# Kernel tuning notes

Measured on AMD Instinct MI355X. Metric: run time of the kernel, lower is better.

The kernel has to match this reference:

```python
import jax, jax.numpy as jnp
import numpy as np

K = 3        # kernel_size
PAD = 1      # padding
STRIDE = 1   # stride (must be 1: module asserts offset HxW == input HxW)
DIL = 1      # dilation


def _bilinear_gather(x, py, px):
    """x: (B,C,H,W); py,px: (B,KK,Ho,Wo) float sample coords.
    Returns (B,C,KK,Ho,Wo), zero outside bounds (DCNv2 semantics)."""
    B, C, H, W = x.shape
    y0 = jnp.floor(py); x0 = jnp.floor(px)
    wy1 = py - y0; wy0 = 1.0 - wy1
    wx1 = px - x0; wx0 = 1.0 - wx1
    flat = x.reshape(B, C, H * W)

    def gather(yi, xi):
        valid = (yi >= 0) & (yi < H) & (xi >= 0) & (xi < W)
        yc = jnp.clip(yi, 0, H - 1).astype(jnp.int32)
        xc = jnp.clip(xi, 0, W - 1).astype(jnp.int32)
        idx = (yc * W + xc).reshape(B, 1, -1)                      # (B,1,KK*Ho*Wo)
        g = jnp.take_along_axis(flat, jnp.broadcast_to(idx, (B, C, idx.shape[-1])), axis=2)
        g = g.reshape(B, C, *yi.shape[1:])                          # (B,C,KK,Ho,Wo)
        return jnp.where(valid[:, None], g, 0.0)

    v00 = gather(y0, x0)
    v01 = gather(y0, x0 + 1)
    v10 = gather(y0 + 1, x0)
    v11 = gather(y0 + 1, x0 + 1)
    wy0 = wy0[:, None]; wy1 = wy1[:, None]; wx0 = wx0[:, None]; wx1 = wx1[:, None]
    return wy0 * (wx0 * v00 + wx1 * v01) + wy1 * (wx0 * v10 + wx1 * v11)


def dcn_v2(x, coord_offset, coord_weight, weight, bias):
    B, C, H, W = x.shape
    O = weight.shape[0]
    KK = K * K
    # offset channels ordered (k, [y,x]) per DCNv2 layout
    offs = coord_offset.reshape(B, KK, 2, H, W)
    oy, ox = offs[:, :, 0], offs[:, :, 1]
    ky, kx = jnp.meshgrid(jnp.arange(K), jnp.arange(K), indexing='ij')
    ky = ky.reshape(KK); kx = kx.reshape(KK)
    # base sampling grid for each output pixel / kernel tap: (KK,H,W)
    py = (jnp.arange(H) * STRIDE - PAD)[None, :, None] + (ky * DIL)[:, None, None]
    px = (jnp.arange(W) * STRIDE - PAD)[None, None, :] + (kx * DIL)[:, None, None]
    py = py.astype(x.dtype)[None] + oy   # (B,KK,H,W)
    px = px.astype(x.dtype)[None] + ox
    sampled = _bilinear_gather(x, py, px)              # (B,C,KK,H,W)
    sampled = sampled * coord_weight[:, None]          # modulation mask
    out = jnp.einsum('bckhw,ock->bohw', sampled, weight.reshape(O, C, KK))
    return out + bias[None, :, None, None]


def setup_inputs() -> dict:
    key = jax.random.key(0)
    k1, k2, k3, k4, k5 = jax.random.split(key, 5)
    B, C, O, H, W = 8, 256, 256, 64, 64
    return {
        'input': jax.random.normal(k1, (B, C, H, W), dtype=jnp.float32),
        'coord_offset': jax.random.normal(k2, (B, 2 * K * K, H, W), dtype=jnp.float32),
        'coord_weight': jax.random.uniform(k3, (B, K * K, H, W), dtype=jnp.float32),
        'weight': jax.random.normal(k4, (O, C, K, K), dtype=jnp.float32) * 0.02,
        'bias': jax.random.normal(k5, (O,), dtype=jnp.float32) * 0.01,
    }


def reference(input, coord_offset, coord_weight, weight, bias):
    return dcn_v2(input, coord_offset, coord_weight, weight, bias)
```

## Files before the change

kernel.cpp:

```cpp
#include <hip/hip_runtime.h>
#include <hip/hip_bf16.h>
#include <stdint.h>

typedef _Float16 f16_t;
typedef f16_t f16x8 __attribute__((ext_vector_type(8)));
typedef float f32x4 __attribute__((ext_vector_type(4)));

__device__ inline void lgkm_barrier() {
    __builtin_amdgcn_s_waitcnt(0xC07F);
    __builtin_amdgcn_s_barrier();
}

__global__ __launch_bounds__(512) void k_prep(const float* __restrict__ x,
                                              const float* __restrict__ w,
                                              f16_t* __restrict__ xt,
                                              f16_t* __restrict__ Wp) {
    __shared__ __align__(16) float lw[9216];
    const int t = threadIdx.x;
    if (blockIdx.x < 512) {
        const int b = blockIdx.x >> 6;
        const int y = blockIdx.x & 63;
        const float* src = x + ((size_t)(b * 256) * 64 + y) * 64;
        const int x4 = (t & 15) * 4;
        const int c0 = (t >> 4) * 8;
        float4 v[8];
#pragma unroll
        for (int e = 0; e < 8; ++e)
            v[e] = *(const float4*)(src + (size_t)(c0 + e) * 4096 + x4);
        f16_t* dst = xt + ((size_t)(b * 64 + y) * 64) * 256;
#pragma unroll
        for (int j = 0; j < 4; ++j) {
            f16x8 o;
#pragma unroll
            for (int e = 0; e < 8; ++e) {
                const float f = (j == 0) ? v[e].x : (j == 1) ? v[e].y
                              : (j == 2) ? v[e].z : v[e].w;
                o[e] = (f16_t)f;
            }
            *(f16x8*)(dst + (x4 + j) * 256 + c0) = o;
        }
    } else {
        const int o0 = (blockIdx.x - 512) * 4;
        const float4* srcw = (const float4*)(w + (size_t)o0 * 2304);
#pragma unroll
        for (int i = 0; i < 5; ++i) {
            const int idx = t + 512 * i;
            if (idx < 2304) ((float4*)lw)[idx] = srcw[idx];
        }
        __syncthreads();
#pragma unroll
        for (int i = 0; i < 3; ++i) {
            const int u = t + 512 * i;
            if (u < 1152) {
                const int o = u / 288, r = u - o * 288;
                const int kb2 = r >> 3, rr = r & 7;
                const int s = rr >> 2, qq = rr & 3;
                const int kk = kb2 >> 2, cp = kb2 & 3;
                f16x8 vv;
#pragma unroll
                for (int e = 0; e < 8; ++e) {
                    const int c = cp * 64 + s * 32 + qq * 8 + e;
                    vv[e] = (f16_t)lw[o * 2304 + c * 9 + kk];
                }
                *(f16x8*)(Wp + ((size_t)(kb2 * 2 + s) * 256 + o0 + o) * 32 + qq * 8) = vv;
            }
        }
    }
}

__global__ __launch_bounds__(512, 4) void k_dcn(
    const f16_t* __restrict__ xt, const f16_t* __restrict__ Wp,
    const float* __restrict__ coff, const float* __restrict__ cwm,
    const float* __restrict__ bias, float* __restrict__ out) {

    __shared__ __align__(16) f16_t sS[2][64 * 64];
    __shared__ __align__(16) int2 sT[9 * 64 * 4];

    const int blk = blockIdx.x;
    const int b  = blk & 7;
    const int h  = blk >> 3;
    const int t = threadIdx.x;
    const int wv = t >> 6;
    const int lane = t & 63;
    const int mg = wv >> 1;
    const int ng = wv & 1;

    const int p = t >> 3;
    const int q = t & 7;

    const int fr = lane & 15;
    const int quad = lane >> 4;
    const int swz = fr & 7;

    for (int u = t; u < 576; u += 512) {
        const int kk = u >> 6, wpx = u & 63;
        float oy = coff[((size_t)(b * 18 + kk * 2 + 0) * 64 + h) * 64 + wpx];
        float ox = coff[((size_t)(b * 18 + kk * 2 + 1) * 64 + h) * 64 + wpx];
        float m  = cwm [((size_t)(b * 9 + kk) * 64 + h) * 64 + wpx];
        float py = (float)(h - 1 + (kk / 3)) + oy;
        float px = (float)(wpx - 1 + (kk % 3)) + ox;
        float fy = floorf(py), fx = floorf(px);
        int y0 = (int)fy, x0 = (int)fx;
        int y1 = y0 + 1,  x1 = x0 + 1;
        float wy1 = py - fy, wx1 = px - fx;
        float wy0 = 1.0f - wy1, wx0 = 1.0f - wx1;
        bool vy0 = (y0 >= 0) && (y0 < 64), vy1 = (y1 >= 0) && (y1 < 64);
        bool vx0 = (x0 >= 0) && (x0 < 64), vx1 = (x1 >= 0) && (x1 < 64);
        int yc0 = min(max(y0, 0), 63), yc1 = min(max(y1, 0), 63);
        int xc0 = min(max(x0, 0), 63), xc1 = min(max(x1, 0), 63);
        const int base = b * 4096;
        float cw[4];
        int   ca[4];
        cw[0] = (vy0 && vx0) ? wy0 * wx0 * m : 0.0f;
        cw[1] = (vy0 && vx1) ? wy0 * wx1 * m : 0.0f;
        cw[2] = (vy1 && vx0) ? wy1 * wx0 * m : 0.0f;
        cw[3] = (vy1 && vx1) ? wy1 * wx1 * m : 0.0f;
        ca[0] = (base + yc0 * 64 + xc0) * 512;
        ca[1] = (base + yc0 * 64 + xc1) * 512;
        ca[2] = (base + yc1 * 64 + xc0) * 512;
        ca[3] = (base + yc1 * 64 + xc1) * 512;
#pragma unroll
        for (int c = 0; c < 4; ++c) {
            unsigned short ws = __builtin_bit_cast(unsigned short, (f16_t)cw[c]);
            sT[(kk * 64 + wpx) * 4 + c] = make_int2(ca[c], (int)ws);
        }
    }
    __syncthreads();

    const f16_t* wA = Wp + (mg * 64 + fr) * 32 + quad * 8;
    f16_t* const swb0 = &sS[0][p * 64 + ((q ^ (p & 7)) * 8)];
    const int qb = q * 16;
    const char* xb = (const char*)xt;

    f32x4 acc[4][2] = {};
    f16x8 aC[4][2];
    f16x8 g0, g1, g2, g3;
    int4 t0, t1;

    auto loadA = [&](int it) {
        const f16_t* wn = wA + (size_t)it * 16384;
#pragma unroll
        for (int mt = 0; mt < 4; ++mt) {
            aC[mt][0] = *(const f16x8*)(wn + mt * 512);
            aC[mt][1] = *(const f16x8*)(wn + 8192 + mt * 512);
        }
    };

    auto gather_issue = [&](int it) {
        const int kk = it >> 2, cp = it & 3;
        const int4* tp = (const int4*)&sT[(kk * 64 + p) * 4];
        t0 = tp[0];
        t1 = tp[1];
        const int cb = cp * 128 + qb;
        g0 = *(const f16x8*)(xb + (t0.x + cb));
        g1 = *(const f16x8*)(xb + (t0.z + cb));
        g2 = *(const f16x8*)(xb + (t1.x + cb));
        g3 = *(const f16x8*)(xb + (t1.z + cb));
    };

    auto combine_write = [&](int buf) {
        f16_t w0 = __builtin_bit_cast(f16_t, (unsigned short)t0.y);
        f16_t w1 = __builtin_bit_cast(f16_t, (unsigned short)t0.w);
        f16_t w2 = __builtin_bit_cast(f16_t, (unsigned short)t1.y);
        f16_t w3 = __builtin_bit_cast(f16_t, (unsigned short)t1.w);
        f16x8 w0v = {w0, w0, w0, w0, w0, w0, w0, w0};
        f16x8 w1v = {w1, w1, w1, w1, w1, w1, w1, w1};
        f16x8 w2v = {w2, w2, w2, w2, w2, w2, w2, w2};
        f16x8 w3v = {w3, w3, w3, w3, w3, w3, w3, w3};
        f16x8 ov = g0 * w0v + g1 * w1v + g2 * w2v + g3 * w3v;
        *(f16x8*)(swb0 + buf * 4096) = ov;
    };

    auto do_mfma = [&](int cur) {
        const f16_t* sb = &sS[cur][ng * 2048];
#pragma unroll
        for (int s = 0; s < 2; ++s) {
            const int coffe = ((s * 4 + quad) ^ swz) * 8;
            f16x8 bb[2];
#pragma unroll
            for (int nt = 0; nt < 2; ++nt)
                bb[nt] = *(const f16x8*)(sb + (nt * 16 + fr) * 64 + coffe);
#pragma unroll
            for (int mt = 0; mt < 4; ++mt)
#pragma unroll
                for (int nt = 0; nt < 2; ++nt)
                    acc[mt][nt] = __builtin_amdgcn_mfma_f32_16x16x32_f16(
                        aC[mt][s], bb[nt], acc[mt][nt], 0, 0, 0);
        }
    };

    gather_issue(0);
    combine_write(0);
    loadA(0);
    lgkm_barrier();

#pragma unroll 2
    for (int it = 0; it < 35; ++it) {
        const int cur = it & 1;
        gather_issue(it + 1);
        __builtin_amdgcn_sched_barrier(0);
        do_mfma(cur);
        __builtin_amdgcn_sched_barrier(0);
        combine_write(1 - cur);
        loadA(it + 1);
        lgkm_barrier();
    }
    do_mfma(1);

    const int rowq = quad * 4;
#pragma unroll
    for (int mt = 0; mt < 4; ++mt) {
#pragma unroll
        for (int r = 0; r < 4; ++r) {
            const int og = mg * 64 + mt * 16 + rowq + r;
            const float bs = bias[og];
            float* opn = out + ((size_t)(b * 256 + og) * 64 + h) * 64 + ng * 32;
#pragma unroll
            for (int nt = 0; nt < 2; ++nt) {
                opn[nt * 16 + fr] = acc[mt][nt][r] + bs;
            }
        }
    }
}

extern "C" void kernel_launch(void* const* d_in, const int* in_sizes, int n_in,
                              void* d_out, int out_size, void* d_ws, size_t ws_size,
                              hipStream_t stream) {
    const float* x    = (const float*)d_in[0];
    const float* coff = (const float*)d_in[1];
    const float* cwm  = (const float*)d_in[2];
    const float* wgt  = (const float*)d_in[3];
    const float* bias = (const float*)d_in[4];
    float* out = (float*)d_out;

    f16_t* xt = (f16_t*)d_ws;
    f16_t* Wp = xt + (size_t)8 * 64 * 64 * 256;

    k_prep<<<576, 512, 0, stream>>>(x, wgt, xt, Wp);
    k_dcn <<<512, 512, 0, stream>>>(xt, Wp, coff, cwm, bias, out);
}
```

Before: 178.8 us.

## Repartition MFMA waves to 32x64 tiles and double-buffer weight registers

Changes the per-wave output tile from 64 output channels by 32 pixels to 32 channels by 64 pixels, so each wave holds half as many weight fragments and reads all four B tiles from shared memory. The loop is manually unrolled by two with ping-pong register sets (aA/aB), so the next weight fragments load before the current MFMAs run. Gather table entries are now reloaded from LDS only once per kernel tap, and MFMA sections get raised wave priority via s_setprio. In exchange, each wave issues more LDS B reads, and the loop tail runs one redundant weight load.

```diff
diff --git a/kernel.cpp b/kernel.cpp
--- a/kernel.cpp
+++ b/kernel.cpp
@@ -82,8 +82,6 @@
     const int t = threadIdx.x;
     const int wv = t >> 6;
     const int lane = t & 63;
-    const int mg = wv >> 1;
-    const int ng = wv & 1;
 
     const int p = t >> 3;
     const int q = t & 7;
@@ -127,30 +125,31 @@
     }
     __syncthreads();
 
-    const f16_t* wA = Wp + (mg * 64 + fr) * 32 + quad * 8;
+    const f16_t* wA = Wp + (wv * 32 + fr) * 32 + quad * 8;
     f16_t* const swb0 = &sS[0][p * 64 + ((q ^ (p & 7)) * 8)];
     const int qb = q * 16;
     const char* xb = (const char*)xt;
 
-    f32x4 acc[4][2] = {};
-    f16x8 aC[4][2];
+    f32x4 acc[2][4] = {};
+    f16x8 aA[2][2], aB[2][2];
     f16x8 g0, g1, g2, g3;
     int4 t0, t1;
 
-    auto loadA = [&](int it) {
+    auto loadA = [&](int it, f16x8 (&a)[2][2]) {
         const f16_t* wn = wA + (size_t)it * 16384;
-#pragma unroll
-        for (int mt = 0; mt < 4; ++mt) {
-            aC[mt][0] = *(const f16x8*)(wn + mt * 512);
-            aC[mt][1] = *(const f16x8*)(wn + 8192 + mt * 512);
-        }
+        a[0][0] = *(const f16x8*)(wn);
+        a[0][1] = *(const f16x8*)(wn + 8192);
+        a[1][0] = *(const f16x8*)(wn + 512);
+        a[1][1] = *(const f16x8*)(wn + 8192 + 512);
     };
 
     auto gather_issue = [&](int it) {
         const int kk = it >> 2, cp = it & 3;
-        const int4* tp = (const int4*)&sT[(kk * 64 + p) * 4];
-        t0 = tp[0];
-        t1 = tp[1];
+        if ((it & 3) == 0) {
+            const int4* tp = (const int4*)&sT[(kk * 64 + p) * 4];
+            t0 = tp[0];
+            t1 = tp[1];
+        }
         const int cb = cp * 128 + qb;
         g0 = *(const f16x8*)(xb + (t0.x + cb));
         g1 = *(const f16x8*)(xb + (t0.z + cb));
@@ -171,52 +170,60 @@
         *(f16x8*)(swb0 + buf * 4096) = ov;
     };
 
-    auto do_mfma = [&](int cur) {
-        const f16_t* sb = &sS[cur][ng * 2048];
+    auto do_mfma = [&](int cur, f16x8 (&a)[2][2]) {
+        const f16_t* sb = &sS[cur][0];
+        __builtin_amdgcn_s_setprio(1);
 #pragma unroll
         for (int s = 0; s < 2; ++s) {
             const int coffe = ((s * 4 + quad) ^ swz) * 8;
-            f16x8 bb[2];
-#pragma unroll
-            for (int nt = 0; nt < 2; ++nt)
+            f16x8 bb[4];
+#pragma unroll
+            for (int nt = 0; nt < 4; ++nt)
                 bb[nt] = *(const f16x8*)(sb + (nt * 16 + fr) * 64 + coffe);
 #pragma unroll
-            for (int mt = 0; mt < 4; ++mt)
-#pragma unroll
-                for (int nt = 0; nt < 2; ++nt)
+            for (int mt = 0; mt < 2; ++mt)
+#pragma unroll
+                for (int nt = 0; nt < 4; ++nt)
                     acc[mt][nt] = __builtin_amdgcn_mfma_f32_16x16x32_f16(
-                        aC[mt][s], bb[nt], acc[mt][nt], 0, 0, 0);
-        }
+                        a[mt][s], bb[nt], acc[mt][nt], 0, 0, 0);
+        }
+        __builtin_amdgcn_s_setprio(0);
     };
 
     gather_issue(0);
     combine_write(0);
-    loadA(0);
+    loadA(0, aA);
     lgkm_barrier();
 
-#pragma unroll 2
-    for (int it = 0; it < 35; ++it) {
-        const int cur = it & 1;
-        gather_issue(it + 1);
-        __builtin_amdgcn_sched_barrier(0);
-        do_mfma(cur);
-        __builtin_amdgcn_sched_barrier(0);
-        combine_write(1 - cur);
-        loadA(it + 1);
+    for (int it2 = 0; it2 < 36; it2 += 2) {
+        gather_issue(it2 + 1);
+        loadA(it2 + 1, aB);
+        __builtin_amdgcn_sched_barrier(0);
+        do_mfma(0, aA);
+        __builtin_amdgcn_sched_barrier(0);
+        combine_write(1);
         lgkm_barrier();
-    }
-    do_mfma(1);
+
+        const bool more = (it2 + 2) < 36;
+        if (more) gather_issue(it2 + 2);
+        loadA(more ? it2 + 2 : 35, aA);
+        __builtin_amdgcn_sched_barrier(0);
+        do_mfma(1, aB);
+        __builtin_amdgcn_sched_barrier(0);
+        if (more) combine_write(0);
+        lgkm_barrier();
+    }
 
     const int rowq = quad * 4;
 #pragma unroll
-    for (int mt = 0; mt < 4; ++mt) {
+    for (int mt = 0; mt < 2; ++mt) {
 #pragma unroll
         for (int r = 0; r < 4; ++r) {
-            const int og = mg * 64 + mt * 16 + rowq + r;
+            const int og = wv * 32 + mt * 16 + rowq + r;
             const float bs = bias[og];
-            float* opn = out + ((size_t)(b * 256 + og) * 64 + h) * 64 + ng * 32;
-#pragma unroll
-            for (int nt = 0; nt < 2; ++nt) {
+            float* opn = out + ((size_t)(b * 256 + og) * 64 + h) * 64;
+#pragma unroll
+            for (int nt = 0; nt < 4; ++nt) {
                 opn[nt * 16 + fr] = acc[mt][nt][r] + bs;
             }
         }
```

Result: faster. 150.3 us (-15.9%).
